# Kernel tuning notes

Hardware: AMD Instinct MI355X
Metric: run time of the kernel (lower is better)

The kernel has to match this reference:

```python
import jax, jax.numpy as jnp
import numpy as np

LAM_U = 0.1
LAM_V = 0.1
LAM_P = 0.1
LAM_Q = 0.1

N_USERS, N_ITEMS, K = 8192, 8192, 256


def _trace(x):
    # PMF repos define trace(x) = sum of squared entries (Frobenius norm^2)
    return jnp.sum(x * x)


def setup_inputs() -> dict:
    key = jax.random.key(0)
    ks = jax.random.split(key, 8)
    R = jax.random.normal(ks[0], (N_USERS, N_ITEMS), jnp.float32)
    R = R * (jax.random.uniform(ks[1], (N_USERS, N_ITEMS)) < 0.05).astype(jnp.float32)
    Y = jax.random.normal(ks[2], (N_USERS, N_ITEMS), jnp.float32)
    Y = Y * (jax.random.uniform(ks[3], (N_USERS, N_ITEMS)) < 0.05).astype(jnp.float32)
    u_features = jax.random.normal(ks[4], (N_USERS, K), jnp.float32)
    v_features = jax.random.normal(ks[5], (N_ITEMS, K), jnp.float32)
    P = jax.random.normal(ks[6], (K, N_USERS), jnp.float32)
    Q = jax.random.normal(ks[7], (K, N_USERS), jnp.float32)
    alpha = jnp.float32(0.5)
    return {"R": R, "u_features": u_features, "v_features": v_features,
            "alpha": alpha, "Y": Y, "P": P, "Q": Q}


def reference(R, u_features, v_features, alpha, Y, P, Q):
    non_zero_mask = (R != 0).astype(jnp.float32)              # [U, I]
    # (P^T * u_features) @ v_features^T : low-rank predicted ratings [U, I]
    predicted = jnp.matmul(P.T * u_features, v_features.T)
    prediction_error = jnp.sum((R - predicted) ** 2 * non_zero_mask) / 2

    non_zero_mask_Y = (Y != 0).astype(jnp.float32)
    predicted_y = jnp.matmul(Q.T * u_features, v_features.T)
    prediction_error_y = alpha * jnp.sum((Y - predicted_y) ** 2 * non_zero_mask_Y) / 2  # computed but NOT returned (faithful to source)

    u_reg = LAM_U * _trace(u_features) / 2
    v_reg = LAM_V * _trace(v_features) / 2
    p_reg = LAM_P * _trace(P) / 2
    q_reg = LAM_Q * _trace(Q) / 2  # computed but not returned (faithful)
    return prediction_error + u_reg + v_reg + p_reg
```

## Files before the change

kernel.cpp:

```cpp
#include <hip/hip_runtime.h>
#include <hip/hip_bf16.h>

typedef __attribute__((ext_vector_type(8))) short short8;
typedef __attribute__((ext_vector_type(4))) float f32x4;

#define N_U 8192
#define N_I 8192
#define KD  256

#define ERR_SLOTS 4096
#define REGA_BASE 4096
#define REGV_BASE 4608
#define SLOTS_END 6656

#define GLD16(g, l) __builtin_amdgcn_global_load_lds( \
    (const __attribute__((address_space(1))) unsigned int*)(unsigned long long)(uintptr_t)(g), \
    (__attribute__((address_space(3))) unsigned int*)(unsigned int)(uintptr_t)(l), 16, 0, 0)

static __device__ __forceinline__ unsigned short f2bf(float x) {
  unsigned u = __builtin_bit_cast(unsigned, x);
  u += 0x7fffu + ((u >> 16) & 1u);
  return (unsigned short)(u >> 16);
}

static __device__ __forceinline__ void block_reduce_store(float v, float* slot) {
  #pragma unroll
  for (int off = 32; off > 0; off >>= 1) v += __shfl_down(v, off, 64);
  __shared__ float red[4];
  int lane = threadIdx.x & 63, wv = threadIdx.x >> 6;
  if (lane == 0) red[wv] = v;
  __syncthreads();
  if (threadIdx.x == 0) *slot = red[0] + red[1] + red[2] + red[3];
}

__global__ __launch_bounds__(256) void pack_a_kernel(
    const float* __restrict__ U, const float* __restrict__ P,
    unsigned short* __restrict__ Abf, float* __restrict__ ws)
{
  __shared__ float Pt[64][65];
  const int u0 = blockIdx.x * 64;
  const int k0 = blockIdx.y * 64;
  const int t = threadIdx.x;
  float ss = 0.f;
  {
    const int ul4 = (t & 15) * 4, klb = t >> 4;
    #pragma unroll
    for (int pass = 0; pass < 4; ++pass) {
      int kl = klb + pass * 16;
      float4 pv = *(const float4*)&P[(size_t)(k0 + kl) * N_U + u0 + ul4];
      Pt[kl][ul4 + 0] = pv.x; Pt[kl][ul4 + 1] = pv.y;
      Pt[kl][ul4 + 2] = pv.z; Pt[kl][ul4 + 3] = pv.w;
      ss += pv.x * pv.x + pv.y * pv.y + pv.z * pv.z + pv.w * pv.w;
    }
  }
  __syncthreads();
  {
    const int k4 = (t & 15) * 4, ulb = t >> 4;
    #pragma unroll
    for (int pass = 0; pass < 4; ++pass) {
      int ul = ulb + pass * 16;
      float4 uv = *(const float4*)&U[(size_t)(u0 + ul) * KD + k0 + k4];
      ss += uv.x * uv.x + uv.y * uv.y + uv.z * uv.z + uv.w * uv.w;
      ushort4 w;
      w.x = f2bf(uv.x * Pt[k4 + 0][ul]);
      w.y = f2bf(uv.y * Pt[k4 + 1][ul]);
      w.z = f2bf(uv.z * Pt[k4 + 2][ul]);
      w.w = f2bf(uv.w * Pt[k4 + 3][ul]);
      *(ushort4*)&Abf[(size_t)(u0 + ul) * KD + k0 + k4] = w;
    }
  }
  block_reduce_store(ss, ws + REGA_BASE + blockIdx.y * 128 + blockIdx.x);
}

__global__ __launch_bounds__(256) void pack_v_kernel(
    const float* __restrict__ V, unsigned short* __restrict__ Vbf,
    float* __restrict__ ws)
{
  size_t i = ((size_t)blockIdx.x * 256 + threadIdx.x) * 4;
  float4 v = *(const float4*)&V[i];
  float ss = v.x * v.x + v.y * v.y + v.z * v.z + v.w * v.w;
  ushort4 w;
  w.x = f2bf(v.x); w.y = f2bf(v.y); w.z = f2bf(v.z); w.w = f2bf(v.w);
  *(ushort4*)&Vbf[i] = w;
  block_reduce_store(ss, ws + REGV_BASE + blockIdx.x);
}

__global__ __launch_bounds__(256) void gemm_loss_kernel(
    const float* __restrict__ R, const unsigned short* __restrict__ Abf,
    const unsigned short* __restrict__ Vbf, float* __restrict__ ws)
{
  __shared__ unsigned short As[128 * 32];
  __shared__ unsigned short Bs[128 * 32];
  const int tid = threadIdx.x;
  const int wv = tid >> 6, lane = tid & 63;
  const int brow = blockIdx.x, bcol = blockIdx.y;
  const int wr = wv >> 1, wc = wv & 1;

  f32x4 acc[4][4] = {};

  const unsigned short* Ag = Abf + (size_t)brow * 128 * KD;
  const unsigned short* Bg = Vbf + (size_t)bcol * 128 * KD;
  const int f0 = wv * 128 + lane;
  const int f1 = f0 + 64;
  const int r0 = lane & 15, kc = (lane >> 4) * 8;

  for (int kt = 0; kt < KD; kt += 32) {
    __syncthreads();
    GLD16(Ag + ((f0 >> 2) * KD + kt + (f0 & 3) * 8), &As[f0 * 8]);
    GLD16(Bg + ((f0 >> 2) * KD + kt + (f0 & 3) * 8), &Bs[f0 * 8]);
    GLD16(Ag + ((f1 >> 2) * KD + kt + (f1 & 3) * 8), &As[f1 * 8]);
    GLD16(Bg + ((f1 >> 2) * KD + kt + (f1 & 3) * 8), &Bs[f1 * 8]);
    __syncthreads();
    short8 a[4], b[4];
    #pragma unroll
    for (int m = 0; m < 4; ++m)
      a[m] = *(const short8*)&As[(wr * 64 + m * 16 + r0) * 32 + kc];
    #pragma unroll
    for (int n = 0; n < 4; ++n)
      b[n] = *(const short8*)&Bs[(wc * 64 + n * 16 + r0) * 32 + kc];
    #pragma unroll
    for (int m = 0; m < 4; ++m)
      #pragma unroll
      for (int n = 0; n < 4; ++n)
        acc[m][n] = __builtin_amdgcn_mfma_f32_16x16x32_bf16(b[n], a[m], acc[m][n], 0, 0, 0);
  }

  float lsum = 0.f;
  const int row0 = brow * 128 + wr * 64 + (lane & 15);
  const size_t col0 = (size_t)bcol * 128 + wc * 64 + (lane >> 4) * 4;
  #pragma unroll
  for (int m = 0; m < 4; ++m) {
    const float* rp = R + (size_t)(row0 + m * 16) * N_I + col0;
    #pragma unroll
    for (int n = 0; n < 4; ++n) {
      float4 rv = *(const float4*)&rp[n * 16];
      if (rv.x != 0.f) { float d = rv.x - acc[m][n][0]; lsum += d * d; }
      if (rv.y != 0.f) { float d = rv.y - acc[m][n][1]; lsum += d * d; }
      if (rv.z != 0.f) { float d = rv.z - acc[m][n][2]; lsum += d * d; }
      if (rv.w != 0.f) { float d = rv.w - acc[m][n][3]; lsum += d * d; }
    }
  }

  #pragma unroll
  for (int off = 32; off > 0; off >>= 1) lsum += __shfl_down(lsum, off, 64);
  float* red = (float*)As;
  __syncthreads();
  if (lane == 0) red[wv] = lsum;
  __syncthreads();
  if (tid == 0) ws[blockIdx.y * 64 + blockIdx.x] = red[0] + red[1] + red[2] + red[3];
}

__global__ __launch_bounds__(256) void finalize_kernel(
    const float* __restrict__ ws, float* __restrict__ out)
{
  __shared__ float sh[256];
  const int tid = threadIdx.x;
  float e = 0.f, r = 0.f;
  for (int i = tid; i < ERR_SLOTS; i += 256) e += ws[i];
  for (int i = REGA_BASE + tid; i < SLOTS_END; i += 256) r += ws[i];
  sh[tid] = 0.5f * e + 0.05f * r;
  __syncthreads();
  #pragma unroll
  for (int s = 128; s > 0; s >>= 1) {
    if (tid < s) sh[tid] += sh[tid + s];
    __syncthreads();
  }
  if (tid == 0) out[0] = sh[0];
}

extern "C" void kernel_launch(void* const* d_in, const int* in_sizes, int n_in,
                              void* d_out, int out_size, void* d_ws, size_t ws_size,
                              hipStream_t stream) {
  const float* R = (const float*)d_in[0];
  const float* U = (const float*)d_in[1];
  const float* V = (const float*)d_in[2];
  const float* P = (const float*)d_in[5];

  float* ws = (float*)d_ws;
  unsigned short* Abf = (unsigned short*)((char*)d_ws + 32768);
  unsigned short* Vbf = Abf + (size_t)N_U * KD;
  float* out = (float*)d_out;

  pack_a_kernel<<<dim3(N_U / 64, KD / 64), 256, 0, stream>>>(U, P, Abf, ws);
  pack_v_kernel<<<dim3((N_I * KD) / (256 * 4)), 256, 0, stream>>>(V, Vbf, ws);
  gemm_loss_kernel<<<dim3(64, 64), 256, 0, stream>>>(R, Abf, Vbf, ws);
  finalize_kernel<<<1, 256, 0, stream>>>(ws, out);
}
```

Baseline: 104.2 us.

## Double-buffer GEMM tiles, shrink N tile to 64, prefetch R during K loop

Moves the GEMM from a 128x128 to a 128x64 block tile, which doubles the grid, and double-buffers the LDS staging so the next K slice loads while MFMAs run on the current one. The R tile values are loaded into registers inside the K loop instead of after it, so their latency hides behind compute. The workspace layout is reorganised to hold twice as many partial-error slots. The price is more A-matrix reloads across blocks and somewhat more register use for the prefetched R values.

```diff
diff --git a/kernel.cpp b/kernel.cpp
--- a/kernel.cpp
+++ b/kernel.cpp
@@ -8,10 +8,10 @@
 #define N_I 8192
 #define KD  256
 
-#define ERR_SLOTS 4096
-#define REGA_BASE 4096
-#define REGV_BASE 4608
-#define SLOTS_END 6656
+#define ERR_SLOTS 8192
+#define REGA_BASE 8192
+#define REGV_BASE 8704
+#define SLOTS_END 10752
 
 #define GLD16(g, l) __builtin_amdgcn_global_load_lds( \
     (const __attribute__((address_space(1))) unsigned int*)(unsigned long long)(uintptr_t)(g), \
@@ -89,56 +89,69 @@
     const float* __restrict__ R, const unsigned short* __restrict__ Abf,
     const unsigned short* __restrict__ Vbf, float* __restrict__ ws)
 {
-  __shared__ unsigned short As[128 * 32];
-  __shared__ unsigned short Bs[128 * 32];
+  __shared__ unsigned short As[2][128 * 32];
+  __shared__ unsigned short Bs[2][64 * 32];
   const int tid = threadIdx.x;
   const int wv = tid >> 6, lane = tid & 63;
   const int brow = blockIdx.x, bcol = blockIdx.y;
   const int wr = wv >> 1, wc = wv & 1;
 
-  f32x4 acc[4][4] = {};
+  f32x4 acc[4][2] = {};
+  float4 rreg[8];
 
   const unsigned short* Ag = Abf + (size_t)brow * 128 * KD;
-  const unsigned short* Bg = Vbf + (size_t)bcol * 128 * KD;
-  const int f0 = wv * 128 + lane;
-  const int f1 = f0 + 64;
+  const unsigned short* Bg = Vbf + (size_t)bcol * 64 * KD;
+  const int fa0 = tid, fa1 = tid + 256, fb = tid;
   const int r0 = lane & 15, kc = (lane >> 4) * 8;
 
-  for (int kt = 0; kt < KD; kt += 32) {
-    __syncthreads();
-    GLD16(Ag + ((f0 >> 2) * KD + kt + (f0 & 3) * 8), &As[f0 * 8]);
-    GLD16(Bg + ((f0 >> 2) * KD + kt + (f0 & 3) * 8), &Bs[f0 * 8]);
-    GLD16(Ag + ((f1 >> 2) * KD + kt + (f1 & 3) * 8), &As[f1 * 8]);
-    GLD16(Bg + ((f1 >> 2) * KD + kt + (f1 & 3) * 8), &Bs[f1 * 8]);
-    __syncthreads();
-    short8 a[4], b[4];
+  const int row0 = brow * 128 + wr * 64 + (lane & 15);
+  const size_t col0 = (size_t)bcol * 64 + wc * 32 + (lane >> 4) * 4;
+  const float* Rtile = R + (size_t)row0 * N_I + col0;
+
+#define STAGE(buf, kt) do { \
+    GLD16(Ag + ((fa0 >> 2) * KD + (kt) + (fa0 & 3) * 8), &As[buf][fa0 * 8]); \
+    GLD16(Ag + ((fa1 >> 2) * KD + (kt) + (fa1 & 3) * 8), &As[buf][fa1 * 8]); \
+    GLD16(Bg + ((fb  >> 2) * KD + (kt) + (fb  & 3) * 8), &Bs[buf][fb * 8]);  \
+  } while (0)
+
+  STAGE(0, 0);
+  asm volatile("s_waitcnt vmcnt(0)" ::: "memory");
+  __builtin_amdgcn_s_barrier();
+
+  #pragma unroll
+  for (int t = 0; t < 8; ++t) {
+    const int cur = t & 1;
+    if (t < 7) STAGE(cur ^ 1, (t + 1) * 32);
+    rreg[t] = *(const float4*)(Rtile + (size_t)((t >> 1) * 16) * N_I + (t & 1) * 16);
+
+    short8 a[4], b[2];
     #pragma unroll
     for (int m = 0; m < 4; ++m)
-      a[m] = *(const short8*)&As[(wr * 64 + m * 16 + r0) * 32 + kc];
-    #pragma unroll
-    for (int n = 0; n < 4; ++n)
-      b[n] = *(const short8*)&Bs[(wc * 64 + n * 16 + r0) * 32 + kc];
+      a[m] = *(const short8*)&As[cur][(wr * 64 + m * 16 + r0) * 32 + kc];
+    #pragma unroll
+    for (int n = 0; n < 2; ++n)
+      b[n] = *(const short8*)&Bs[cur][(wc * 32 + n * 16 + r0) * 32 + kc];
     #pragma unroll
     for (int m = 0; m < 4; ++m)
       #pragma unroll
-      for (int n = 0; n < 4; ++n)
+      for (int n = 0; n < 2; ++n)
         acc[m][n] = __builtin_amdgcn_mfma_f32_16x16x32_bf16(b[n], a[m], acc[m][n], 0, 0, 0);
-  }
-
+
+    asm volatile("s_waitcnt lgkmcnt(0) vmcnt(1)" ::: "memory");
+    __builtin_amdgcn_s_barrier();
+  }
+#undef STAGE
+
+  asm volatile("s_waitcnt vmcnt(0)" ::: "memory");
   float lsum = 0.f;
-  const int row0 = brow * 128 + wr * 64 + (lane & 15);
-  const size_t col0 = (size_t)bcol * 128 + wc * 64 + (lane >> 4) * 4;
-  #pragma unroll
-  for (int m = 0; m < 4; ++m) {
-    const float* rp = R + (size_t)(row0 + m * 16) * N_I + col0;
-    #pragma unroll
-    for (int n = 0; n < 4; ++n) {
-      float4 rv = *(const float4*)&rp[n * 16];
-      if (rv.x != 0.f) { float d = rv.x - acc[m][n][0]; lsum += d * d; }
-      if (rv.y != 0.f) { float d = rv.y - acc[m][n][1]; lsum += d * d; }
-      if (rv.z != 0.f) { float d = rv.z - acc[m][n][2]; lsum += d * d; }
-      if (rv.w != 0.f) { float d = rv.w - acc[m][n][3]; lsum += d * d; }
-    }
+  #pragma unroll
+  for (int t = 0; t < 8; ++t) {
+    const int m = t >> 1, n = t & 1;
+    float4 rv = rreg[t];
+    if (rv.x != 0.f) { float d = rv.x - acc[m][n][0]; lsum += d * d; }
+    if (rv.y != 0.f) { float d = rv.y - acc[m][n][1]; lsum += d * d; }
+    if (rv.z != 0.f) { float d = rv.z - acc[m][n][2]; lsum += d * d; }
+    if (rv.w != 0.f) { float d = rv.w - acc[m][n][3]; lsum += d * d; }
   }
 
   #pragma unroll
@@ -176,13 +189,13 @@
   const float* V = (const float*)d_in[2];
   const float* P = (const float*)d_in[5];
 
-  float* ws = (float*)d_ws;
-  unsigned short* Abf = (unsigned short*)((char*)d_ws + 32768);
+  unsigned short* Abf = (unsigned short*)d_ws;
   unsigned short* Vbf = Abf + (size_t)N_U * KD;
+  float* ws = (float*)((char*)d_ws + 2 * 4194304);
   float* out = (float*)d_out;
 
   pack_a_kernel<<<dim3(N_U / 64, KD / 64), 256, 0, stream>>>(U, P, Abf, ws);
   pack_v_kernel<<<dim3((N_I * KD) / (256 * 4)), 256, 0, stream>>>(V, Vbf, ws);
-  gemm_loss_kernel<<<dim3(64, 64), 256, 0, stream>>>(R, Abf, Vbf, ws);
+  gemm_loss_kernel<<<dim3(64, 128), 256, 0, stream>>>(R, Abf, Vbf, ws);
   finalize_kernel<<<1, 256, 0, stream>>>(ws, out);
 }
```

Result: slower. 128.9 us (+23.7%).

## Load GEMM operands directly from global into registers, drop LDS staging

Applied to the files above, without the earlier changes.

The GEMM kernel no longer stages A and B tiles through shared memory with global_load_lds and barriers. Each wave now loads its MFMA fragments straight from global memory (served by L1/L2), with the k-loop fully unrolled and an occupancy hint of three blocks per SM. All R tile loads are issued together before the masked error computation, and each wave writes its own partial sum instead of doing a block reduction, which enlarges the workspace slot area. This removes barriers and LDS traffic but repeats global/L2 reads across waves, since operand reuse now relies on the cache.

```diff
diff --git a/kernel.cpp b/kernel.cpp
--- a/kernel.cpp
+++ b/kernel.cpp
@@ -8,14 +8,10 @@
 #define N_I 8192
 #define KD  256
 
-#define ERR_SLOTS 4096
-#define REGA_BASE 4096
-#define REGV_BASE 4608
-#define SLOTS_END 6656
-
-#define GLD16(g, l) __builtin_amdgcn_global_load_lds( \
-    (const __attribute__((address_space(1))) unsigned int*)(unsigned long long)(uintptr_t)(g), \
-    (__attribute__((address_space(3))) unsigned int*)(unsigned int)(uintptr_t)(l), 16, 0, 0)
+#define ERR_SLOTS 16384
+#define REGA_BASE 16384
+#define REGV_BASE 16896
+#define SLOTS_END 18944
 
 static __device__ __forceinline__ unsigned short f2bf(float x) {
   unsigned u = __builtin_bit_cast(unsigned, x);
@@ -85,39 +81,34 @@
   block_reduce_store(ss, ws + REGV_BASE + blockIdx.x);
 }
 
-__global__ __launch_bounds__(256) void gemm_loss_kernel(
+__global__ __launch_bounds__(256, 3) void gemm_loss_kernel(
     const float* __restrict__ R, const unsigned short* __restrict__ Abf,
     const unsigned short* __restrict__ Vbf, float* __restrict__ ws)
 {
-  __shared__ unsigned short As[128 * 32];
-  __shared__ unsigned short Bs[128 * 32];
   const int tid = threadIdx.x;
   const int wv = tid >> 6, lane = tid & 63;
   const int brow = blockIdx.x, bcol = blockIdx.y;
   const int wr = wv >> 1, wc = wv & 1;
 
+  const int trow = brow * 128 + wr * 64;
+  const int tcol = bcol * 128 + wc * 64;
+
+  const int r0 = lane & 15, kc = (lane >> 4) * 8;
+
+  const unsigned short* Ab = Abf + (size_t)(trow + r0) * KD + kc;
+  const unsigned short* Bb = Vbf + (size_t)(tcol + r0) * KD + kc;
+
   f32x4 acc[4][4] = {};
 
-  const unsigned short* Ag = Abf + (size_t)brow * 128 * KD;
-  const unsigned short* Bg = Vbf + (size_t)bcol * 128 * KD;
-  const int f0 = wv * 128 + lane;
-  const int f1 = f0 + 64;
-  const int r0 = lane & 15, kc = (lane >> 4) * 8;
-
+  #pragma unroll
   for (int kt = 0; kt < KD; kt += 32) {
-    __syncthreads();
-    GLD16(Ag + ((f0 >> 2) * KD + kt + (f0 & 3) * 8), &As[f0 * 8]);
-    GLD16(Bg + ((f0 >> 2) * KD + kt + (f0 & 3) * 8), &Bs[f0 * 8]);
-    GLD16(Ag + ((f1 >> 2) * KD + kt + (f1 & 3) * 8), &As[f1 * 8]);
-    GLD16(Bg + ((f1 >> 2) * KD + kt + (f1 & 3) * 8), &Bs[f1 * 8]);
-    __syncthreads();
     short8 a[4], b[4];
     #pragma unroll
     for (int m = 0; m < 4; ++m)
-      a[m] = *(const short8*)&As[(wr * 64 + m * 16 + r0) * 32 + kc];
+      a[m] = *(const short8*)(Ab + (size_t)(m * 16) * KD + kt);
     #pragma unroll
     for (int n = 0; n < 4; ++n)
-      b[n] = *(const short8*)&Bs[(wc * 64 + n * 16 + r0) * 32 + kc];
+      b[n] = *(const short8*)(Bb + (size_t)(n * 16) * KD + kt);
     #pragma unroll
     for (int m = 0; m < 4; ++m)
       #pragma unroll
@@ -125,29 +116,30 @@
         acc[m][n] = __builtin_amdgcn_mfma_f32_16x16x32_bf16(b[n], a[m], acc[m][n], 0, 0, 0);
   }
 
+  const float* Rt = R + (size_t)(trow + r0) * N_I + tcol + (lane >> 4) * 4;
+  float4 rv[4][4];
+  #pragma unroll
+  for (int m = 0; m < 4; ++m)
+    #pragma unroll
+    for (int n = 0; n < 4; ++n)
+      rv[m][n] = *(const float4*)(Rt + (size_t)(m * 16) * N_I + n * 16);
+
   float lsum = 0.f;
-  const int row0 = brow * 128 + wr * 64 + (lane & 15);
-  const size_t col0 = (size_t)bcol * 128 + wc * 64 + (lane >> 4) * 4;
   #pragma unroll
   for (int m = 0; m < 4; ++m) {
-    const float* rp = R + (size_t)(row0 + m * 16) * N_I + col0;
     #pragma unroll
     for (int n = 0; n < 4; ++n) {
-      float4 rv = *(const float4*)&rp[n * 16];
-      if (rv.x != 0.f) { float d = rv.x - acc[m][n][0]; lsum += d * d; }
-      if (rv.y != 0.f) { float d = rv.y - acc[m][n][1]; lsum += d * d; }
-      if (rv.z != 0.f) { float d = rv.z - acc[m][n][2]; lsum += d * d; }
-      if (rv.w != 0.f) { float d = rv.w - acc[m][n][3]; lsum += d * d; }
+      if (rv[m][n].x != 0.f) { float d = rv[m][n].x - acc[m][n][0]; lsum += d * d; }
+      if (rv[m][n].y != 0.f) { float d = rv[m][n].y - acc[m][n][1]; lsum += d * d; }
+      if (rv[m][n].z != 0.f) { float d = rv[m][n].z - acc[m][n][2]; lsum += d * d; }
+      if (rv[m][n].w != 0.f) { float d = rv[m][n].w - acc[m][n][3]; lsum += d * d; }
     }
   }
 
   #pragma unroll
   for (int off = 32; off > 0; off >>= 1) lsum += __shfl_down(lsum, off, 64);
-  float* red = (float*)As;
-  __syncthreads();
-  if (lane == 0) red[wv] = lsum;
-  __syncthreads();
-  if (tid == 0) ws[blockIdx.y * 64 + blockIdx.x] = red[0] + red[1] + red[2] + red[3];
+  if (lane == 0)
+    ws[((blockIdx.y * 64 + blockIdx.x) << 2) | wv] = lsum;
 }
 
 __global__ __launch_bounds__(256) void finalize_kernel(
@@ -176,9 +168,9 @@
   const float* V = (const float*)d_in[2];
   const float* P = (const float*)d_in[5];
 
-  float* ws = (float*)d_ws;
-  unsigned short* Abf = (unsigned short*)((char*)d_ws + 32768);
+  unsigned short* Abf = (unsigned short*)d_ws;
   unsigned short* Vbf = Abf + (size_t)N_U * KD;
+  float* ws = (float*)((char*)d_ws + 2 * 4194304);
   float* out = (float*)d_out;
 
   pack_a_kernel<<<dim3(N_U / 64, KD / 64), 256, 0, stream>>>(U, P, Abf, ws);
```

New measurement: 210.4 us. +101.9%, slower.

## Double-buffer LDS tiles and XOR-swizzle K chunks in GEMM loss kernel

Applied to the files above, without the earlier changes.

Splits the shared A/B tiles into two buffers so global-to-LDS loads for the next K step run while MFMAs use the current one, with one barrier per step instead of two. Adds an XOR swizzle on the 16-byte K chunks to reduce LDS bank conflicts on the fragment reads. Moves the packed bf16 buffers to a 1MB workspace offset. This doubles LDS use per block, which may lower occupancy.

```diff
diff --git a/kernel.cpp b/kernel.cpp
--- a/kernel.cpp
+++ b/kernel.cpp
@@ -89,8 +89,8 @@
     const float* __restrict__ R, const unsigned short* __restrict__ Abf,
     const unsigned short* __restrict__ Vbf, float* __restrict__ ws)
 {
-  __shared__ unsigned short As[128 * 32];
-  __shared__ unsigned short Bs[128 * 32];
+  __shared__ unsigned short As[2][128 * 32];
+  __shared__ unsigned short Bs[2][128 * 32];
   const int tid = threadIdx.x;
   const int wv = tid >> 6, lane = tid & 63;
   const int brow = blockIdx.x, bcol = blockIdx.y;
@@ -102,22 +102,51 @@
   const unsigned short* Bg = Vbf + (size_t)bcol * 128 * KD;
   const int f0 = wv * 128 + lane;
   const int f1 = f0 + 64;
-  const int r0 = lane & 15, kc = (lane >> 4) * 8;
-
-  for (int kt = 0; kt < KD; kt += 32) {
-    __syncthreads();
-    GLD16(Ag + ((f0 >> 2) * KD + kt + (f0 & 3) * 8), &As[f0 * 8]);
-    GLD16(Bg + ((f0 >> 2) * KD + kt + (f0 & 3) * 8), &Bs[f0 * 8]);
-    GLD16(Ag + ((f1 >> 2) * KD + kt + (f1 & 3) * 8), &As[f1 * 8]);
-    GLD16(Bg + ((f1 >> 2) * KD + kt + (f1 & 3) * 8), &Bs[f1 * 8]);
-    __syncthreads();
+  const int sw0 = (((f0 & 3) ^ ((f0 >> 3) & 3)) * 8);
+  const int sw1 = (((f1 & 3) ^ ((f1 >> 3) & 3)) * 8);
+  const int r0 = lane & 15;
+  const int kq = ((lane >> 4) ^ ((r0 >> 1) & 3)) * 8;
+
+#define STAGE(buf, kt) do { \
+    GLD16(Ag + ((f0 >> 2) * KD + (kt)) + sw0, &As[buf][f0 * 8]); \
+    GLD16(Bg + ((f0 >> 2) * KD + (kt)) + sw0, &Bs[buf][f0 * 8]); \
+    GLD16(Ag + ((f1 >> 2) * KD + (kt)) + sw1, &As[buf][f1 * 8]); \
+    GLD16(Bg + ((f1 >> 2) * KD + (kt)) + sw1, &Bs[buf][f1 * 8]); \
+  } while (0)
+
+  STAGE(0, 0);
+  asm volatile("s_waitcnt vmcnt(0)" ::: "memory");
+  __builtin_amdgcn_s_barrier();
+
+  #pragma unroll
+  for (int t = 0; t < 7; ++t) {
+    const int cur = t & 1;
+    STAGE(cur ^ 1, (t + 1) * 32);
     short8 a[4], b[4];
     #pragma unroll
     for (int m = 0; m < 4; ++m)
-      a[m] = *(const short8*)&As[(wr * 64 + m * 16 + r0) * 32 + kc];
+      a[m] = *(const short8*)&As[cur][(wr * 64 + m * 16 + r0) * 32 + kq];
     #pragma unroll
     for (int n = 0; n < 4; ++n)
-      b[n] = *(const short8*)&Bs[(wc * 64 + n * 16 + r0) * 32 + kc];
+      b[n] = *(const short8*)&Bs[cur][(wc * 64 + n * 16 + r0) * 32 + kq];
+    #pragma unroll
+    for (int m = 0; m < 4; ++m)
+      #pragma unroll
+      for (int n = 0; n < 4; ++n)
+        acc[m][n] = __builtin_amdgcn_mfma_f32_16x16x32_bf16(b[n], a[m], acc[m][n], 0, 0, 0);
+    asm volatile("s_waitcnt vmcnt(0)" ::: "memory");
+    __builtin_amdgcn_s_barrier();
+  }
+#undef STAGE
+
+  {
+    short8 a[4], b[4];
+    #pragma unroll
+    for (int m = 0; m < 4; ++m)
+      a[m] = *(const short8*)&As[1][(wr * 64 + m * 16 + r0) * 32 + kq];
+    #pragma unroll
+    for (int n = 0; n < 4; ++n)
+      b[n] = *(const short8*)&Bs[1][(wc * 64 + n * 16 + r0) * 32 + kq];
     #pragma unroll
     for (int m = 0; m < 4; ++m)
       #pragma unroll
@@ -177,7 +206,7 @@
   const float* P = (const float*)d_in[5];
 
   float* ws = (float*)d_ws;
-  unsigned short* Abf = (unsigned short*)((char*)d_ws + 32768);
+  unsigned short* Abf = (unsigned short*)((char*)d_ws + (1 << 20));
   unsigned short* Vbf = Abf + (size_t)N_U * KD;
   float* out = (float*)d_out;
 
```

Measured after the change: 103.5 us. No clear change (-0.7%).
